# Performance work log

Measured on AMD Instinct MI355X. Metric: run time of the kernel, lower is better.

Reference implementation:

```python
import jax, jax.numpy as jnp
import numpy as np

B, D_IN, J = 65536, 512, 8
HIDDEN = [256, 128, 64]


def setup_inputs() -> dict:
    key = jax.random.key(0)
    ks = jax.random.split(key, 8)
    dims = [D_IN] + HIDDEN
    inp = {
        "x": jax.random.normal(ks[0], (B, D_IN), dtype=jnp.float32),
        # soft domain indicator (one-hot in practice; math is a weighted sum either way)
        "domain_indicator": jax.random.uniform(ks[1], (B, J), dtype=jnp.float32),
    }
    for i in range(3):
        fin, fout = dims[i], dims[i + 1]
        scale = (2.0 / (fin + fout)) ** 0.5  # glorot_normal
        inp[f"sk{i}"] = jax.random.normal(ks[2 + i], (fin, fout), dtype=jnp.float32) * scale
        inp[f"sb{i}"] = jnp.zeros((fout,), dtype=jnp.float32)
        inp[f"dk{i}"] = jax.random.normal(ks[5 + i], (J, fin, fout), dtype=jnp.float32) * scale
        inp[f"db{i}"] = jnp.zeros((J, fout), dtype=jnp.float32)
    return inp


def _star_forward(x, domain_indicator, layers):
    # layer 0: x is [B, D]; fused shared*domain weights -> batched per-domain GEMM
    sk, sb, dk, db = layers[0]
    w = sk[None] * dk                                   # [J, D, H0]
    h = jnp.einsum('bi,jio->bjo', x, w) + (sb[None] + db)[None]  # [B, J, H0]
    h = jax.nn.relu(h)
    for sk, sb, dk, db in layers[1:]:
        w = sk[None] * dk                               # [J, Hi, Hi+1]
        h = jnp.einsum('bji,jio->bjo', h, w) + (sb[None] + db)[None]
        h = jax.nn.relu(h)
    # select/mix domains: sum_j h[b,j,:] * indicator[b,j]
    return jnp.einsum('bjo,bj->bo', h, domain_indicator)


def reference(x, domain_indicator, sk0, sb0, dk0, db0, sk1, sb1, dk1, db1, sk2, sb2, dk2, db2):
    layers = [(sk0, sb0, dk0, db0), (sk1, sb1, dk1, db1), (sk2, sb2, dk2, db2)]
    return _star_forward(x, domain_indicator, layers)
```

## Files before the change

kernel.cpp:

```cpp
#include <hip/hip_runtime.h>
#include <stdint.h>


namespace {

typedef __attribute__((ext_vector_type(8))) short bf16x8;
typedef __attribute__((ext_vector_type(4))) float f32x4;

union Frag { bf16x8 v; unsigned int u[4]; };

constexpr size_t WS_L0   = 0;
constexpr size_t WS_L1   = 4194304;
constexpr size_t WS_L2   = 5242880;
constexpr size_t WS_B0   = 5505024;
constexpr size_t WS_B1   = 5513216;
constexpr size_t WS_B2   = 5517312;
constexpr size_t WS_X    = 5519360;
constexpr size_t WS_TOTAL_BIG = WS_X + (size_t)65536 * 2048;

constexpr int PREP_TOTAL = 1048576 + 262144 + 65536 + 2048 + 1024 + 512;

__device__ __forceinline__ void splitpair(float a, float b,
                                          unsigned int& hi, unsigned int& lo) {
    unsigned int ua = __float_as_uint(a);
    unsigned int ub = __float_as_uint(b);
    unsigned int ha = ua & 0xffff0000u;
    unsigned int hb = ub & 0xffff0000u;
    float ra = a - __uint_as_float(ha);
    float rb = b - __uint_as_float(hb);
    hi = (ua >> 16) | hb;
    lo = (__float_as_uint(ra) >> 16) | (__float_as_uint(rb) & 0xffff0000u);
}

__device__ __forceinline__ void split16(float v, unsigned short& h, unsigned short& l) {
    unsigned int u = __float_as_uint(v);
    h = (unsigned short)(u >> 16);
    float r = v - __uint_as_float(u & 0xffff0000u);
    l = (unsigned short)(__float_as_uint(r) >> 16);
}

__device__ __forceinline__ unsigned int packsplit(float v) {
    unsigned int u = __float_as_uint(v);
    unsigned int h = u & 0xffff0000u;
    float r = v - __uint_as_float(h);
    return h | (__float_as_uint(r) >> 16);
}

__device__ __forceinline__ void unpack2(unsigned int e0, unsigned int e1,
                                        unsigned int& hi, unsigned int& lo) {
    hi = (e0 >> 16) | (e1 & 0xffff0000u);
    lo = (e0 & 0xffffu) | (e1 << 16);
}

__global__ void prep_ws(const float* __restrict__ sk0, const float* __restrict__ dk0,
                        const float* __restrict__ sk1, const float* __restrict__ dk1,
                        const float* __restrict__ sk2, const float* __restrict__ dk2,
                        const float* __restrict__ sb0, const float* __restrict__ db0,
                        const float* __restrict__ sb1, const float* __restrict__ db1,
                        const float* __restrict__ sb2, const float* __restrict__ db2,
                        char* __restrict__ ws) {
    int tid = blockIdx.x * 256 + threadIdx.x;
    if (tid < 1048576) {
        int n = tid & 255, k = (tid >> 8) & 511, j = tid >> 17;
        float wv = sk0[k * 256 + n] * dk0[(size_t)(j * 512 + k) * 256 + n];
        unsigned int u = __float_as_uint(wv);
        unsigned int h = u & 0xffff0000u;
        float r = wv - __uint_as_float(h);
        int pair = (j * 16 + (k >> 5)) * 16 + (n >> 4);
        int lane = (n & 15) | (((k >> 3) & 3) << 4);
        size_t off = WS_L0 + (size_t)pair * 2048 + lane * 16 + (k & 7) * 2;
        *(unsigned short*)(ws + off)        = (unsigned short)(u >> 16);
        *(unsigned short*)(ws + off + 1024) = (unsigned short)(__float_as_uint(r) >> 16);
    } else if (tid < 1310720) {
        int t = tid - 1048576;
        int n = t & 127, k = (t >> 7) & 255, j = t >> 15;
        float wv = sk1[k * 128 + n] * dk1[(size_t)(j * 256 + k) * 128 + n];
        unsigned int u = __float_as_uint(wv);
        unsigned int h = u & 0xffff0000u;
        float r = wv - __uint_as_float(h);
        int pair = (j * 8 + (k >> 5)) * 8 + (n >> 4);
        int lane = (n & 15) | (((k >> 3) & 3) << 4);
        size_t off = WS_L1 + (size_t)pair * 2048 + lane * 16 + (k & 7) * 2;
        *(unsigned short*)(ws + off)        = (unsigned short)(u >> 16);
        *(unsigned short*)(ws + off + 1024) = (unsigned short)(__float_as_uint(r) >> 16);
    } else if (tid < 1376256) {
        int t = tid - 1310720;
        int n = t & 63, k = (t >> 6) & 127, j = t >> 13;
        float wv = sk2[k * 64 + n] * dk2[(size_t)(j * 128 + k) * 64 + n];
        unsigned int u = __float_as_uint(wv);
        unsigned int h = u & 0xffff0000u;
        float r = wv - __uint_as_float(h);
        int pair = (j * 4 + (k >> 5)) * 4 + (n >> 4);
        int lane = (n & 15) | (((k >> 3) & 3) << 4);
        size_t off = WS_L2 + (size_t)pair * 2048 + lane * 16 + (k & 7) * 2;
        *(unsigned short*)(ws + off)        = (unsigned short)(u >> 16);
        *(unsigned short*)(ws + off + 1024) = (unsigned short)(__float_as_uint(r) >> 16);
    } else if (tid < 1378304) {
        int t = tid - 1376256;
        ((float*)(ws + WS_B0))[t] = sb0[t & 255] + db0[t];
    } else if (tid < 1379328) {
        int t = tid - 1378304;
        ((float*)(ws + WS_B1))[t] = sb1[t & 127] + db1[t];
    } else if (tid < PREP_TOTAL) {
        int t = tid - 1379328;
        ((float*)(ws + WS_B2))[t] = sb2[t & 63] + db2[t];
    }
}

__global__ __launch_bounds__(256) void prep_xsplit(const float* __restrict__ x,
                                                   char* __restrict__ ws) {
    __shared__ __align__(16) unsigned int xf[8192];
    const int b     = blockIdx.x;
    const int tid   = threadIdx.x;
    const int row16 = tid >> 4;
    const int seg   = tid & 15;

    const float* src = x + ((size_t)b * 16 + row16) * 512 + seg * 32;
    float4 a[8];
#pragma unroll
    for (int i = 0; i < 8; ++i) a[i] = *(const float4*)(src + i * 4);

    unsigned int hi[16], lo[16];
#pragma unroll
    for (int i = 0; i < 8; ++i) {
        splitpair(a[i].x, a[i].y, hi[2 * i],     lo[2 * i]);
        splitpair(a[i].z, a[i].w, hi[2 * i + 1], lo[2 * i + 1]);
    }
#pragma unroll
    for (int qq = 0; qq < 4; ++qq) {
        const int lane = row16 | (qq << 4);
        const int di = seg * 512 + lane * 4;
        uint4 vh = { hi[qq * 4 + 0], hi[qq * 4 + 1], hi[qq * 4 + 2], hi[qq * 4 + 3] };
        uint4 vl = { lo[qq * 4 + 0], lo[qq * 4 + 1], lo[qq * 4 + 2], lo[qq * 4 + 3] };
        *(uint4*)&xf[di]       = vh;
        *(uint4*)&xf[di + 256] = vl;
    }
    __syncthreads();

    uint4* dst = (uint4*)(ws + WS_X + (size_t)b * 32768) + tid * 8;
#pragma unroll
    for (int i = 0; i < 8; ++i) dst[i] = *(const uint4*)&xf[tid * 32 + i * 4];
}

__global__ __launch_bounds__(512, 4) void star_mfma_v8(
    const float* __restrict__ ind,
    const char* __restrict__ ws,
    float* __restrict__ out)
{
    __shared__ __align__(16) char smem[67584];
    unsigned short* const H0hi = (unsigned short*)smem;
    unsigned short* const H0lo = (unsigned short*)(smem + 33792);
    unsigned short* const H1hi = (unsigned short*)smem;
    unsigned short* const H1lo = (unsigned short*)(smem + 33792);
    __shared__ float indS[8 * 65];

    const int tid  = threadIdx.x;
    const int w    = tid >> 6;
    const int lane = tid & 63;
    const int c    = lane & 15;
    const int q    = lane >> 4;
    const int bx   = blockIdx.x;
    const int b0   = bx * 64;
    const int mh   = w >> 2;
    const int nt2  = w & 3;

    const char* xp  = ws + WS_X;
    const char* wB0 = ws + WS_L0;
    const char* wB1 = ws + WS_L1;
    const char* wB2 = ws + WS_L2;
    const float* bias0 = (const float*)(ws + WS_B0);
    const float* bias1 = (const float*)(ws + WS_B1);
    const float* bias2 = (const float*)(ws + WS_B2);

    indS[(tid & 7) * 65 + (tid >> 3)] = ind[(size_t)b0 * 8 + tid];

    const f32x4 z = {0.f, 0.f, 0.f, 0.f};
    f32x4 oacc[2]; oacc[0] = z; oacc[1] = z;

    __syncthreads();

    for (int jp = 0; jp < 4; ++jp) {
        f32x4 acc0[2][4][2];
#pragma unroll
        for (int jj = 0; jj < 2; ++jj)
#pragma unroll
            for (int mt = 0; mt < 4; ++mt)
#pragma unroll
                for (int ntl = 0; ntl < 2; ++ntl) acc0[jj][mt][ntl] = z;

        for (int kc = 0; kc < 16; ++kc) {
            Frag Ahi[4], Alo[4];
#pragma unroll
            for (int mt = 0; mt < 4; ++mt) {
                const char* ap = xp + ((size_t)((bx * 4 + mt) * 16 + kc) * 2048) + lane * 16;
                *(uint4*)Ahi[mt].u = *(const uint4*)ap;
                *(uint4*)Alo[mt].u = *(const uint4*)(ap + 1024);
            }
#pragma unroll
            for (int jj = 0; jj < 2; ++jj) {
                const int j = jp * 2 + jj;
#pragma unroll
                for (int ntl = 0; ntl < 2; ++ntl) {
                    const int nt = w * 2 + ntl;
                    const char* pb = wB0 + ((size_t)((j * 16 + kc) * 16 + nt) * 2048) + lane * 16;
                    Frag Bhi, Blo;
                    *(uint4*)Bhi.u = *(const uint4*)pb;
                    *(uint4*)Blo.u = *(const uint4*)(pb + 1024);
#pragma unroll
                    for (int mt = 0; mt < 4; ++mt) {
                        acc0[jj][mt][ntl] = __builtin_amdgcn_mfma_f32_16x16x32_bf16(Ahi[mt].v, Bhi.v, acc0[jj][mt][ntl], 0, 0, 0);
                        acc0[jj][mt][ntl] = __builtin_amdgcn_mfma_f32_16x16x32_bf16(Ahi[mt].v, Blo.v, acc0[jj][mt][ntl], 0, 0, 0);
                        acc0[jj][mt][ntl] = __builtin_amdgcn_mfma_f32_16x16x32_bf16(Alo[mt].v, Bhi.v, acc0[jj][mt][ntl], 0, 0, 0);
                    }
                }
            }
        }

#pragma unroll
        for (int jj = 0; jj < 2; ++jj) {
            const int j = jp * 2 + jj;

#pragma unroll
            for (int ntl = 0; ntl < 2; ++ntl) {
                const int k = w * 32 + ntl * 16 + c;
                const float bv = bias0[j * 256 + k];
#pragma unroll
                for (int mt = 0; mt < 4; ++mt)
#pragma unroll
                    for (int r = 0; r < 4; ++r) {
                        float v = fmaxf(acc0[jj][mt][ntl][r] + bv, 0.f);
                        unsigned short h16, l16;
                        split16(v, h16, l16);
                        const int idx = (mt * 16 + q * 4 + r) * 264 + k;
                        H0hi[idx] = h16;
                        H0lo[idx] = l16;
                    }
            }
            __syncthreads();

            f32x4 acc1[4];
#pragma unroll
            for (int mt = 0; mt < 4; ++mt) acc1[mt] = z;
            for (int kc = 0; kc < 8; ++kc) {
                Frag Ahi[4], Alo[4];
#pragma unroll
                for (int mt = 0; mt < 4; ++mt) {
                    const int idx = (mt * 16 + c) * 264 + kc * 32 + q * 8;
                    *(uint4*)Ahi[mt].u = *(const uint4*)&H0hi[idx];
                    *(uint4*)Alo[mt].u = *(const uint4*)&H0lo[idx];
                }
                const char* pb = wB1 + ((size_t)((j * 8 + kc) * 8 + w) * 2048) + lane * 16;
                Frag Bhi, Blo;
                *(uint4*)Bhi.u = *(const uint4*)pb;
                *(uint4*)Blo.u = *(const uint4*)(pb + 1024);
#pragma unroll
                for (int mt = 0; mt < 4; ++mt) {
                    acc1[mt] = __builtin_amdgcn_mfma_f32_16x16x32_bf16(Ahi[mt].v, Bhi.v, acc1[mt], 0, 0, 0);
                    acc1[mt] = __builtin_amdgcn_mfma_f32_16x16x32_bf16(Ahi[mt].v, Blo.v, acc1[mt], 0, 0, 0);
                    acc1[mt] = __builtin_amdgcn_mfma_f32_16x16x32_bf16(Alo[mt].v, Bhi.v, acc1[mt], 0, 0, 0);
                }
            }
            __syncthreads();

            {
                const int k = w * 16 + c;
                const float bv = bias1[j * 128 + k];
#pragma unroll
                for (int mt = 0; mt < 4; ++mt)
#pragma unroll
                    for (int r = 0; r < 4; ++r) {
                        float v = fmaxf(acc1[mt][r] + bv, 0.f);
                        unsigned short h16, l16;
                        split16(v, h16, l16);
                        const int idx = (mt * 16 + q * 4 + r) * 136 + k;
                        H1hi[idx] = h16;
                        H1lo[idx] = l16;
                    }
            }
            __syncthreads();

            f32x4 acc2[2]; acc2[0] = z; acc2[1] = z;
            for (int kc = 0; kc < 4; ++kc) {
                const char* pb = wB2 + ((size_t)((j * 4 + kc) * 4 + nt2) * 2048) + lane * 16;
                Frag Bhi, Blo;
                *(uint4*)Bhi.u = *(const uint4*)pb;
                *(uint4*)Blo.u = *(const uint4*)(pb + 1024);
#pragma unroll
                for (int mtl = 0; mtl < 2; ++mtl) {
                    Frag Ahi, Alo;
                    const int idx = ((mh * 2 + mtl) * 16 + c) * 136 + kc * 32 + q * 8;
                    *(uint4*)Ahi.u = *(const uint4*)&H1hi[idx];
                    *(uint4*)Alo.u = *(const uint4*)&H1lo[idx];
                    acc2[mtl] = __builtin_amdgcn_mfma_f32_16x16x32_bf16(Ahi.v, Bhi.v, acc2[mtl], 0, 0, 0);
                    acc2[mtl] = __builtin_amdgcn_mfma_f32_16x16x32_bf16(Ahi.v, Blo.v, acc2[mtl], 0, 0, 0);
                    acc2[mtl] = __builtin_amdgcn_mfma_f32_16x16x32_bf16(Alo.v, Bhi.v, acc2[mtl], 0, 0, 0);
                }
            }
            {
                const float bv = bias2[j * 64 + nt2 * 16 + c];
#pragma unroll
                for (int mtl = 0; mtl < 2; ++mtl)
#pragma unroll
                    for (int r = 0; r < 4; ++r) {
                        float v = fmaxf(acc2[mtl][r] + bv, 0.f);
                        const int m = (mh * 2 + mtl) * 16 + q * 4 + r;
                        oacc[mtl][r] = fmaf(indS[j * 65 + m], v, oacc[mtl][r]);
                    }
            }
            __syncthreads();
        }
    }

#pragma unroll
    for (int mtl = 0; mtl < 2; ++mtl)
#pragma unroll
        for (int r = 0; r < 4; ++r)
            out[(size_t)(b0 + (mh * 2 + mtl) * 16 + q * 4 + r) * 64 + nt2 * 16 + c] = oacc[mtl][r];
}

__global__ __launch_bounds__(256, 3) void star_mfma_fb(
    const float* __restrict__ x,
    const float* __restrict__ ind,
    const char* __restrict__ ws,
    float* __restrict__ out)
{
    __shared__ unsigned int H0s[32 * 260];
    __shared__ unsigned int H1s[32 * 132];
    __shared__ float indS[8 * 33];

    const int tid  = threadIdx.x;
    const int w    = tid >> 6;
    const int lane = tid & 63;
    const int c    = lane & 15;
    const int q    = lane >> 4;
    const int b0   = blockIdx.x * 32;

    const char* wB0 = ws + WS_L0;
    const char* wB1 = ws + WS_L1;
    const char* wB2 = ws + WS_L2;
    const float* bias0 = (const float*)(ws + WS_B0);
    const float* bias1 = (const float*)(ws + WS_B1);
    const float* bias2 = (const float*)(ws + WS_B2);

    indS[(tid & 7) * 33 + (tid >> 3)] = ind[(size_t)b0 * 8 + tid];

    const f32x4 z = {0.f, 0.f, 0.f, 0.f};
    f32x4 oacc[2]; oacc[0] = z; oacc[1] = z;

    __syncthreads();

    for (int j = 0; j < 8; ++j) {
        f32x4 acc0[2][4];
#pragma unroll
        for (int mt = 0; mt < 2; ++mt)
#pragma unroll
            for (int ntl = 0; ntl < 4; ++ntl) acc0[mt][ntl] = z;

        for (int kc = 0; kc < 16; ++kc) {
            Frag Ahi[2], Alo[2];
#pragma unroll
            for (int mt = 0; mt < 2; ++mt) {
                const float* ap = x + (size_t)(b0 + mt * 16 + c) * 512 + kc * 32 + q * 8;
                float4 a0 = *(const float4*)ap;
                float4 a1 = *(const float4*)(ap + 4);
                splitpair(a0.x, a0.y, Ahi[mt].u[0], Alo[mt].u[0]);
                splitpair(a0.z, a0.w, Ahi[mt].u[1], Alo[mt].u[1]);
                splitpair(a1.x, a1.y, Ahi[mt].u[2], Alo[mt].u[2]);
                splitpair(a1.z, a1.w, Ahi[mt].u[3], Alo[mt].u[3]);
            }
#pragma unroll
            for (int ntl = 0; ntl < 4; ++ntl) {
                const int nt = w * 4 + ntl;
                const char* pb = wB0 + ((size_t)((j * 16 + kc) * 16 + nt) * 2048) + lane * 16;
                Frag Bhi, Blo;
                *(uint4*)Bhi.u = *(const uint4*)pb;
                *(uint4*)Blo.u = *(const uint4*)(pb + 1024);
#pragma unroll
                for (int mt = 0; mt < 2; ++mt) {
                    acc0[mt][ntl] = __builtin_amdgcn_mfma_f32_16x16x32_bf16(Ahi[mt].v, Bhi.v, acc0[mt][ntl], 0, 0, 0);
                    acc0[mt][ntl] = __builtin_amdgcn_mfma_f32_16x16x32_bf16(Ahi[mt].v, Blo.v, acc0[mt][ntl], 0, 0, 0);
                    acc0[mt][ntl] = __builtin_amdgcn_mfma_f32_16x16x32_bf16(Alo[mt].v, Bhi.v, acc0[mt][ntl], 0, 0, 0);
                }
            }
        }
#pragma unroll
        for (int ntl = 0; ntl < 4; ++ntl) {
            const float bv = bias0[j * 256 + w * 64 + ntl * 16 + c];
#pragma unroll
            for (int mt = 0; mt < 2; ++mt)
#pragma unroll
                for (int r = 0; r < 4; ++r) {
                    float v = acc0[mt][ntl][r] + bv;
                    v = fmaxf(v, 0.f);
                    H0s[(mt * 16 + q * 4 + r) * 260 + w * 64 + ntl * 16 + c] = packsplit(v);
                }
        }
        __syncthreads();

        f32x4 acc1[2][2];
#pragma unroll
        for (int mt = 0; mt < 2; ++mt)
#pragma unroll
            for (int ntl = 0; ntl < 2; ++ntl) acc1[mt][ntl] = z;

        for (int kc = 0; kc < 8; ++kc) {
            Frag Ahi[2], Alo[2];
#pragma unroll
            for (int mt = 0; mt < 2; ++mt) {
                const unsigned int* hp = &H0s[(mt * 16 + c) * 260 + kc * 32 + q * 8];
                uint4 e0 = *(const uint4*)hp;
                uint4 e1 = *(const uint4*)(hp + 4);
                unpack2(e0.x, e0.y, Ahi[mt].u[0], Alo[mt].u[0]);
                unpack2(e0.z, e0.w, Ahi[mt].u[1], Alo[mt].u[1]);
                unpack2(e1.x, e1.y, Ahi[mt].u[2], Alo[mt].u[2]);
                unpack2(e1.z, e1.w, Ahi[mt].u[3], Alo[mt].u[3]);
            }
#pragma unroll
            for (int ntl = 0; ntl < 2; ++ntl) {
                const int nt = w * 2 + ntl;
                const char* pb = wB1 + ((size_t)((j * 8 + kc) * 8 + nt) * 2048) + lane * 16;
                Frag Bhi, Blo;
                *(uint4*)Bhi.u = *(const uint4*)pb;
                *(uint4*)Blo.u = *(const uint4*)(pb + 1024);
#pragma unroll
                for (int mt = 0; mt < 2; ++mt) {
                    acc1[mt][ntl] = __builtin_amdgcn_mfma_f32_16x16x32_bf16(Ahi[mt].v, Bhi.v, acc1[mt][ntl], 0, 0, 0);
                    acc1[mt][ntl] = __builtin_amdgcn_mfma_f32_16x16x32_bf16(Ahi[mt].v, Blo.v, acc1[mt][ntl], 0, 0, 0);
                    acc1[mt][ntl] = __builtin_amdgcn_mfma_f32_16x16x32_bf16(Alo[mt].v, Bhi.v, acc1[mt][ntl], 0, 0, 0);
                }
            }
        }
#pragma unroll
        for (int ntl = 0; ntl < 2; ++ntl) {
            const float bv = bias1[j * 128 + w * 32 + ntl * 16 + c];
#pragma unroll
            for (int mt = 0; mt < 2; ++mt)
#pragma unroll
                for (int r = 0; r < 4; ++r) {
                    float v = acc1[mt][ntl][r] + bv;
                    v = fmaxf(v, 0.f);
                    H1s[(mt * 16 + q * 4 + r) * 132 + w * 32 + ntl * 16 + c] = packsplit(v);
                }
        }
        __syncthreads();

        f32x4 acc2[2]; acc2[0] = z; acc2[1] = z;

        for (int kc = 0; kc < 4; ++kc) {
            Frag Ahi[2], Alo[2];
#pragma unroll
            for (int mt = 0; mt < 2; ++mt) {
                const unsigned int* hp = &H1s[(mt * 16 + c) * 132 + kc * 32 + q * 8];
                uint4 e0 = *(const uint4*)hp;
                uint4 e1 = *(const uint4*)(hp + 4);
                unpack2(e0.x, e0.y, Ahi[mt].u[0], Alo[mt].u[0]);
                unpack2(e0.z, e0.w, Ahi[mt].u[1], Alo[mt].u[1]);
                unpack2(e1.x, e1.y, Ahi[mt].u[2], Alo[mt].u[2]);
                unpack2(e1.z, e1.w, Ahi[mt].u[3], Alo[mt].u[3]);
            }
            const char* pb = wB2 + ((size_t)((j * 4 + kc) * 4 + w) * 2048) + lane * 16;
            Frag Bhi, Blo;
            *(uint4*)Bhi.u = *(const uint4*)pb;
            *(uint4*)Blo.u = *(const uint4*)(pb + 1024);
#pragma unroll
            for (int mt = 0; mt < 2; ++mt) {
                acc2[mt] = __builtin_amdgcn_mfma_f32_16x16x32_bf16(Ahi[mt].v, Bhi.v, acc2[mt], 0, 0, 0);
                acc2[mt] = __builtin_amdgcn_mfma_f32_16x16x32_bf16(Ahi[mt].v, Blo.v, acc2[mt], 0, 0, 0);
                acc2[mt] = __builtin_amdgcn_mfma_f32_16x16x32_bf16(Alo[mt].v, Bhi.v, acc2[mt], 0, 0, 0);
            }
        }
        {
            const float bv = bias2[j * 64 + w * 16 + c];
#pragma unroll
            for (int mt = 0; mt < 2; ++mt)
#pragma unroll
                for (int r = 0; r < 4; ++r) {
                    float v = acc2[mt][r] + bv;
                    v = fmaxf(v, 0.f);
                    oacc[mt][r] = fmaf(indS[j * 33 + mt * 16 + q * 4 + r], v, oacc[mt][r]);
                }
        }
    }

#pragma unroll
    for (int mt = 0; mt < 2; ++mt)
#pragma unroll
        for (int r = 0; r < 4; ++r)
            out[(size_t)(b0 + mt * 16 + q * 4 + r) * 64 + w * 16 + c] = oacc[mt][r];
}

}

extern "C" void kernel_launch(void* const* d_in, const int* in_sizes, int n_in,
                              void* d_out, int out_size, void* d_ws, size_t ws_size,
                              hipStream_t stream) {
    const float* x   = (const float*)d_in[0];
    const float* ind = (const float*)d_in[1];
    const float* sk0 = (const float*)d_in[2];
    const float* sb0 = (const float*)d_in[3];
    const float* dk0 = (const float*)d_in[4];
    const float* db0 = (const float*)d_in[5];
    const float* sk1 = (const float*)d_in[6];
    const float* sb1 = (const float*)d_in[7];
    const float* dk1 = (const float*)d_in[8];
    const float* db1 = (const float*)d_in[9];
    const float* sk2 = (const float*)d_in[10];
    const float* sb2 = (const float*)d_in[11];
    const float* dk2 = (const float*)d_in[12];
    const float* db2 = (const float*)d_in[13];
    char* ws   = (char*)d_ws;
    float* out = (float*)d_out;

    prep_ws<<<dim3((PREP_TOTAL + 255) / 256), dim3(256), 0, stream>>>(
        sk0, dk0, sk1, dk1, sk2, dk2, sb0, db0, sb1, db1, sb2, db2, ws);

    if (ws_size >= WS_TOTAL_BIG) {
        prep_xsplit<<<dim3(4096), dim3(256), 0, stream>>>(x, ws);
        star_mfma_v8<<<dim3(1024), dim3(512), 0, stream>>>(ind, ws, out);
    } else {
        star_mfma_fb<<<dim3(2048), dim3(256), 0, stream>>>(x, ind, ws, out);
    }
}
```

Measured before the change: 776.8 us.

## Switch layer-0 GEMM to 32x32x16 MFMA and merge prep kernels

Layer 0 now uses 32x32x16 bf16 MFMA tiles instead of 16x16x32. The pre-split x and weight workspace layouts are rebuilt to match the 32-wide fragment shape, and the epilogue row and column mapping is rewritten for the 16-element accumulators. The weight prep and x-split kernels are merged into one launch, which removes a launch and lets the two prep phases overlap. Larger MFMA tiles mean fewer fragment loads per FLOP, at the cost of more accumulator registers and different per-instruction latency.

Measured after the change: 1.694 ms. +118.1%, slower.

```diff
diff --git a/kernel.cpp b/kernel.cpp
--- a/kernel.cpp
+++ b/kernel.cpp
@@ -6,6 +6,7 @@
 
 typedef __attribute__((ext_vector_type(8))) short bf16x8;
 typedef __attribute__((ext_vector_type(4))) float f32x4;
+typedef __attribute__((ext_vector_type(16))) float f32x16;
 
 union Frag { bf16x8 v; unsigned int u[4]; };
 
@@ -18,7 +19,9 @@
 constexpr size_t WS_X    = 5519360;
 constexpr size_t WS_TOTAL_BIG = WS_X + (size_t)65536 * 2048;
 
-constexpr int PREP_TOTAL = 1048576 + 262144 + 65536 + 2048 + 1024 + 512;
+constexpr int PREP_TOTAL  = 1048576 + 262144 + 65536 + 2048 + 1024 + 512;
+constexpr int NB_WSPREP   = PREP_TOTAL / 256;
+constexpr int NB_XSPLIT   = 2048;
 
 __device__ __forceinline__ void splitpair(float a, float b,
                                           unsigned int& hi, unsigned int& lo) {
@@ -52,97 +55,102 @@
     lo = (e0 & 0xffffu) | (e1 << 16);
 }
 
-__global__ void prep_ws(const float* __restrict__ sk0, const float* __restrict__ dk0,
-                        const float* __restrict__ sk1, const float* __restrict__ dk1,
-                        const float* __restrict__ sk2, const float* __restrict__ dk2,
-                        const float* __restrict__ sb0, const float* __restrict__ db0,
-                        const float* __restrict__ sb1, const float* __restrict__ db1,
-                        const float* __restrict__ sb2, const float* __restrict__ db2,
-                        char* __restrict__ ws) {
-    int tid = blockIdx.x * 256 + threadIdx.x;
-    if (tid < 1048576) {
-        int n = tid & 255, k = (tid >> 8) & 511, j = tid >> 17;
-        float wv = sk0[k * 256 + n] * dk0[(size_t)(j * 512 + k) * 256 + n];
-        unsigned int u = __float_as_uint(wv);
-        unsigned int h = u & 0xffff0000u;
-        float r = wv - __uint_as_float(h);
-        int pair = (j * 16 + (k >> 5)) * 16 + (n >> 4);
-        int lane = (n & 15) | (((k >> 3) & 3) << 4);
-        size_t off = WS_L0 + (size_t)pair * 2048 + lane * 16 + (k & 7) * 2;
-        *(unsigned short*)(ws + off)        = (unsigned short)(u >> 16);
-        *(unsigned short*)(ws + off + 1024) = (unsigned short)(__float_as_uint(r) >> 16);
-    } else if (tid < 1310720) {
-        int t = tid - 1048576;
-        int n = t & 127, k = (t >> 7) & 255, j = t >> 15;
-        float wv = sk1[k * 128 + n] * dk1[(size_t)(j * 256 + k) * 128 + n];
-        unsigned int u = __float_as_uint(wv);
-        unsigned int h = u & 0xffff0000u;
-        float r = wv - __uint_as_float(h);
-        int pair = (j * 8 + (k >> 5)) * 8 + (n >> 4);
-        int lane = (n & 15) | (((k >> 3) & 3) << 4);
-        size_t off = WS_L1 + (size_t)pair * 2048 + lane * 16 + (k & 7) * 2;
-        *(unsigned short*)(ws + off)        = (unsigned short)(u >> 16);
-        *(unsigned short*)(ws + off + 1024) = (unsigned short)(__float_as_uint(r) >> 16);
-    } else if (tid < 1376256) {
-        int t = tid - 1310720;
-        int n = t & 63, k = (t >> 6) & 127, j = t >> 13;
-        float wv = sk2[k * 64 + n] * dk2[(size_t)(j * 128 + k) * 64 + n];
-        unsigned int u = __float_as_uint(wv);
-        unsigned int h = u & 0xffff0000u;
-        float r = wv - __uint_as_float(h);
-        int pair = (j * 4 + (k >> 5)) * 4 + (n >> 4);
-        int lane = (n & 15) | (((k >> 3) & 3) << 4);
-        size_t off = WS_L2 + (size_t)pair * 2048 + lane * 16 + (k & 7) * 2;
-        *(unsigned short*)(ws + off)        = (unsigned short)(u >> 16);
-        *(unsigned short*)(ws + off + 1024) = (unsigned short)(__float_as_uint(r) >> 16);
-    } else if (tid < 1378304) {
-        int t = tid - 1376256;
-        ((float*)(ws + WS_B0))[t] = sb0[t & 255] + db0[t];
-    } else if (tid < 1379328) {
-        int t = tid - 1378304;
-        ((float*)(ws + WS_B1))[t] = sb1[t & 127] + db1[t];
-    } else if (tid < PREP_TOTAL) {
-        int t = tid - 1379328;
-        ((float*)(ws + WS_B2))[t] = sb2[t & 63] + db2[t];
+__global__ __launch_bounds__(256) void prep_all(
+        const float* __restrict__ sk0, const float* __restrict__ dk0,
+        const float* __restrict__ sk1, const float* __restrict__ dk1,
+        const float* __restrict__ sk2, const float* __restrict__ dk2,
+        const float* __restrict__ sb0, const float* __restrict__ db0,
+        const float* __restrict__ sb1, const float* __restrict__ db1,
+        const float* __restrict__ sb2, const float* __restrict__ db2,
+        const float* __restrict__ x, char* __restrict__ ws, int use32) {
+    __shared__ __align__(16) unsigned int xf[8192];
+
+    if (blockIdx.x < NB_WSPREP) {
+        int tid = blockIdx.x * 256 + threadIdx.x;
+        if (tid < 1048576) {
+            int n = tid & 255, k = (tid >> 8) & 511, j = tid >> 17;
+            float wv = sk0[k * 256 + n] * dk0[(size_t)(j * 512 + k) * 256 + n];
+            unsigned int u = __float_as_uint(wv);
+            unsigned int h = u & 0xffff0000u;
+            float r = wv - __uint_as_float(h);
+            int pair, lane;
+            if (use32) {
+                pair = (j * 32 + (k >> 4)) * 8 + (n >> 5);
+                lane = (n & 31) | (((k >> 3) & 1) << 5);
+            } else {
+                pair = (j * 16 + (k >> 5)) * 16 + (n >> 4);
+                lane = (n & 15) | (((k >> 3) & 3) << 4);
+            }
+            size_t off = WS_L0 + (size_t)pair * 2048 + lane * 16 + (k & 7) * 2;
+            *(unsigned short*)(ws + off)        = (unsigned short)(u >> 16);
+            *(unsigned short*)(ws + off + 1024) = (unsigned short)(__float_as_uint(r) >> 16);
+        } else if (tid < 1310720) {
+            int t = tid - 1048576;
+            int n = t & 127, k = (t >> 7) & 255, j = t >> 15;
+            float wv = sk1[k * 128 + n] * dk1[(size_t)(j * 256 + k) * 128 + n];
+            unsigned int u = __float_as_uint(wv);
+            unsigned int h = u & 0xffff0000u;
+            float r = wv - __uint_as_float(h);
+            int pair = (j * 8 + (k >> 5)) * 8 + (n >> 4);
+            int lane = (n & 15) | (((k >> 3) & 3) << 4);
+            size_t off = WS_L1 + (size_t)pair * 2048 + lane * 16 + (k & 7) * 2;
+            *(unsigned short*)(ws + off)        = (unsigned short)(u >> 16);
+            *(unsigned short*)(ws + off + 1024) = (unsigned short)(__float_as_uint(r) >> 16);
+        } else if (tid < 1376256) {
+            int t = tid - 1310720;
+            int n = t & 63, k = (t >> 6) & 127, j = t >> 13;
+            float wv = sk2[k * 64 + n] * dk2[(size_t)(j * 128 + k) * 64 + n];
+            unsigned int u = __float_as_uint(wv);
+            unsigned int h = u & 0xffff0000u;
+            float r = wv - __uint_as_float(h);
+            int pair = (j * 4 + (k >> 5)) * 4 + (n >> 4);
+            int lane = (n & 15) | (((k >> 3) & 3) << 4);
+            size_t off = WS_L2 + (size_t)pair * 2048 + lane * 16 + (k & 7) * 2;
+            *(unsigned short*)(ws + off)        = (unsigned short)(u >> 16);
+            *(unsigned short*)(ws + off + 1024) = (unsigned short)(__float_as_uint(r) >> 16);
+        } else if (tid < 1378304) {
+            int t = tid - 1376256;
+            ((float*)(ws + WS_B0))[t] = sb0[t & 255] + db0[t];
+        } else if (tid < 1379328) {
+            int t = tid - 1378304;
+            ((float*)(ws + WS_B1))[t] = sb1[t & 127] + db1[t];
+        } else if (tid < PREP_TOTAL) {
+            int t = tid - 1379328;
+            ((float*)(ws + WS_B2))[t] = sb2[t & 63] + db2[t];
+        }
+    } else {
+        const int b   = blockIdx.x - NB_WSPREP;
+        const int tid = threadIdx.x;
+        for (int p = 0; p < 2; ++p) {
+            if (p) __syncthreads();
+#pragma unroll
+            for (int i = 0; i < 4; ++i) {
+                const int f  = i * 256 + tid;
+                const int r  = f >> 5;
+                const int gl = f & 31;
+                const float* src = x + ((size_t)b * 32 + r) * 512 + p * 256 + gl * 8;
+                float4 a0 = *(const float4*)src;
+                float4 a1 = *(const float4*)(src + 4);
+                unsigned int hi[4], lo[4];
+                splitpair(a0.x, a0.y, hi[0], lo[0]);
+                splitpair(a0.z, a0.w, hi[1], lo[1]);
+                splitpair(a1.x, a1.y, hi[2], lo[2]);
+                splitpair(a1.z, a1.w, hi[3], lo[3]);
+                const int kcl  = gl >> 1;
+                const int lane = r | ((gl & 1) << 5);
+                const int di   = kcl * 512 + lane * 4;
+                *(uint4*)&xf[di]       = *(uint4*)hi;
+                *(uint4*)&xf[di + 256] = *(uint4*)lo;
+            }
+            __syncthreads();
+            uint4* dst = (uint4*)(ws + WS_X + (size_t)b * 65536 + (size_t)p * 32768) + tid * 8;
+#pragma unroll
+            for (int i = 0; i < 8; ++i) dst[i] = *(const uint4*)&xf[tid * 32 + i * 4];
+        }
     }
 }
 
-__global__ __launch_bounds__(256) void prep_xsplit(const float* __restrict__ x,
-                                                   char* __restrict__ ws) {
-    __shared__ __align__(16) unsigned int xf[8192];
-    const int b     = blockIdx.x;
-    const int tid   = threadIdx.x;
-    const int row16 = tid >> 4;
-    const int seg   = tid & 15;
-
-    const float* src = x + ((size_t)b * 16 + row16) * 512 + seg * 32;
-    float4 a[8];
-#pragma unroll
-    for (int i = 0; i < 8; ++i) a[i] = *(const float4*)(src + i * 4);
-
-    unsigned int hi[16], lo[16];
-#pragma unroll
-    for (int i = 0; i < 8; ++i) {
-        splitpair(a[i].x, a[i].y, hi[2 * i],     lo[2 * i]);
-        splitpair(a[i].z, a[i].w, hi[2 * i + 1], lo[2 * i + 1]);
-    }
-#pragma unroll
-    for (int qq = 0; qq < 4; ++qq) {
-        const int lane = row16 | (qq << 4);
-        const int di = seg * 512 + lane * 4;
-        uint4 vh = { hi[qq * 4 + 0], hi[qq * 4 + 1], hi[qq * 4 + 2], hi[qq * 4 + 3] };
-        uint4 vl = { lo[qq * 4 + 0], lo[qq * 4 + 1], lo[qq * 4 + 2], lo[qq * 4 + 3] };
-        *(uint4*)&xf[di]       = vh;
-        *(uint4*)&xf[di + 256] = vl;
-    }
-    __syncthreads();
-
-    uint4* dst = (uint4*)(ws + WS_X + (size_t)b * 32768) + tid * 8;
-#pragma unroll
-    for (int i = 0; i < 8; ++i) dst[i] = *(const uint4*)&xf[tid * 32 + i * 4];
-}
-
-__global__ __launch_bounds__(512, 4) void star_mfma_v8(
+__global__ __launch_bounds__(512, 4) void star_mfma_v9(
     const float* __restrict__ ind,
     const char* __restrict__ ws,
     float* __restrict__ out)
@@ -159,6 +167,8 @@
     const int lane = tid & 63;
     const int c    = lane & 15;
     const int q    = lane >> 4;
+    const int l31  = lane & 31;
+    const int lh   = lane >> 5;
     const int bx   = blockIdx.x;
     const int b0   = bx * 64;
     const int mh   = w >> 2;
@@ -175,43 +185,39 @@
     indS[(tid & 7) * 65 + (tid >> 3)] = ind[(size_t)b0 * 8 + tid];
 
     const f32x4 z = {0.f, 0.f, 0.f, 0.f};
+    const f32x16 z16 = {0.f, 0.f, 0.f, 0.f, 0.f, 0.f, 0.f, 0.f,
+                        0.f, 0.f, 0.f, 0.f, 0.f, 0.f, 0.f, 0.f};
     f32x4 oacc[2]; oacc[0] = z; oacc[1] = z;
 
     __syncthreads();
 
     for (int jp = 0; jp < 4; ++jp) {
-        f32x4 acc0[2][4][2];
+        f32x16 acc0[2][2];
 #pragma unroll
         for (int jj = 0; jj < 2; ++jj)
 #pragma unroll
-            for (int mt = 0; mt < 4; ++mt)
-#pragma unroll
-                for (int ntl = 0; ntl < 2; ++ntl) acc0[jj][mt][ntl] = z;
-
-        for (int kc = 0; kc < 16; ++kc) {
-            Frag Ahi[4], Alo[4];
-#pragma unroll
-            for (int mt = 0; mt < 4; ++mt) {
-                const char* ap = xp + ((size_t)((bx * 4 + mt) * 16 + kc) * 2048) + lane * 16;
+            for (int mt = 0; mt < 2; ++mt) acc0[jj][mt] = z16;
+
+        for (int kc = 0; kc < 32; ++kc) {
+            Frag Ahi[2], Alo[2];
+#pragma unroll
+            for (int mt = 0; mt < 2; ++mt) {
+                const char* ap = xp + ((size_t)((bx * 2 + mt) * 32 + kc) * 2048) + lane * 16;
                 *(uint4*)Ahi[mt].u = *(const uint4*)ap;
                 *(uint4*)Alo[mt].u = *(const uint4*)(ap + 1024);
             }
 #pragma unroll
             for (int jj = 0; jj < 2; ++jj) {
                 const int j = jp * 2 + jj;
-#pragma unroll
-                for (int ntl = 0; ntl < 2; ++ntl) {
-                    const int nt = w * 2 + ntl;
-                    const char* pb = wB0 + ((size_t)((j * 16 + kc) * 16 + nt) * 2048) + lane * 16;
-                    Frag Bhi, Blo;
-                    *(uint4*)Bhi.u = *(const uint4*)pb;
-                    *(uint4*)Blo.u = *(const uint4*)(pb + 1024);
-#pragma unroll
-                    for (int mt = 0; mt < 4; ++mt) {
-                        acc0[jj][mt][ntl] = __builtin_amdgcn_mfma_f32_16x16x32_bf16(Ahi[mt].v, Bhi.v, acc0[jj][mt][ntl], 0, 0, 0);
-                        acc0[jj][mt][ntl] = __builtin_amdgcn_mfma_f32_16x16x32_bf16(Ahi[mt].v, Blo.v, acc0[jj][mt][ntl], 0, 0, 0);
-                        acc0[jj][mt][ntl] = __builtin_amdgcn_mfma_f32_16x16x32_bf16(Alo[mt].v, Bhi.v, acc0[jj][mt][ntl], 0, 0, 0);
-                    }
+                const char* pb = wB0 + ((size_t)((j * 32 + kc) * 8 + w) * 2048) + lane * 16;
+                Frag Bhi, Blo;
+                *(uint4*)Bhi.u = *(const uint4*)pb;
+                *(uint4*)Blo.u = *(const uint4*)(pb + 1024);
+#pragma unroll
+                for (int mt = 0; mt < 2; ++mt) {
+                    acc0[jj][mt] = __builtin_amdgcn_mfma_f32_32x32x16_bf16(Ahi[mt].v, Bhi.v, acc0[jj][mt], 0, 0, 0);
+                    acc0[jj][mt] = __builtin_amdgcn_mfma_f32_32x32x16_bf16(Ahi[mt].v, Blo.v, acc0[jj][mt], 0, 0, 0);
+                    acc0[jj][mt] = __builtin_amdgcn_mfma_f32_32x32x16_bf16(Alo[mt].v, Bhi.v, acc0[jj][mt], 0, 0, 0);
                 }
             }
         }
@@ -220,18 +226,19 @@
         for (int jj = 0; jj < 2; ++jj) {
             const int j = jp * 2 + jj;
 
-#pragma unroll
-            for (int ntl = 0; ntl < 2; ++ntl) {
-                const int k = w * 32 + ntl * 16 + c;
-                const float bv = bias0[j * 256 + k];
-#pragma unroll
-                for (int mt = 0; mt < 4; ++mt)
-#pragma unroll
-                    for (int r = 0; r < 4; ++r) {
-                        float v = fmaxf(acc0[jj][mt][ntl][r] + bv, 0.f);
+            {
+                const int col = w * 32 + l31;
+                const float bv = bias0[j * 256 + col];
+                const int rb = 4 * lh;
+#pragma unroll
+                for (int mt = 0; mt < 2; ++mt)
+#pragma unroll
+                    for (int r = 0; r < 16; ++r) {
+                        const int row = mt * 32 + (r & 3) + 8 * (r >> 2) + rb;
+                        float v = fmaxf(acc0[jj][mt][r] + bv, 0.f);
                         unsigned short h16, l16;
                         split16(v, h16, l16);
-                        const int idx = (mt * 16 + q * 4 + r) * 264 + k;
+                        const int idx = row * 264 + col;
                         H0hi[idx] = h16;
                         H0lo[idx] = l16;
                     }
@@ -511,13 +518,15 @@
     char* ws   = (char*)d_ws;
     float* out = (float*)d_out;
 
-    prep_ws<<<dim3((PREP_TOTAL + 255) / 256), dim3(256), 0, stream>>>(
-        sk0, dk0, sk1, dk1, sk2, dk2, sb0, db0, sb1, db1, sb2, db2, ws);
-
     if (ws_size >= WS_TOTAL_BIG) {
-        prep_xsplit<<<dim3(4096), dim3(256), 0, stream>>>(x, ws);
-        star_mfma_v8<<<dim3(1024), dim3(512), 0, stream>>>(ind, ws, out);
+        prep_all<<<dim3(NB_WSPREP + NB_XSPLIT), dim3(256), 0, stream>>>(
+            sk0, dk0, sk1, dk1, sk2, dk2, sb0, db0, sb1, db1, sb2, db2,
+            x, ws, 1);
+        star_mfma_v9<<<dim3(1024), dim3(512), 0, stream>>>(ind, ws, out);
     } else {
+        prep_all<<<dim3(NB_WSPREP), dim3(256), 0, stream>>>(
+            sk0, dk0, sk1, dk1, sk2, dk2, sb0, db0, sb1, db1, sb2, db2,
+            x, ws, 0);
         star_mfma_fb<<<dim3(2048), dim3(256), 0, stream>>>(x, ind, ws, out);
     }
 }
```
